# Kernel tuning notes

Measured on AMD Instinct MI355X. Metric: run time of the kernel, lower is better.

The kernel has to match this reference:

```python
import jax, jax.numpy as jnp
import numpy as np

N, E, F, H, HEADS, G = 50000, 800000, 128, 128, 4, 512
BN_EPS = 1e-5

def setup_inputs() -> dict:
    key = jax.random.key(0)
    ks = jax.random.split(key, 12)
    x = jax.random.normal(ks[0], (N, F), jnp.float32)
    edge_index = jax.random.randint(ks[1], (2, E), 0, N, jnp.int64)
    batch = jnp.sort(jax.random.randint(ks[2], (N,), 0, G, jnp.int64))
    w_gcn = jax.random.normal(ks[3], (F, H), jnp.float32) * 0.09
    b_gcn = jnp.zeros((H,), jnp.float32)
    g2_gamma = jnp.ones((H,), jnp.float32); g2_beta = jnp.zeros((H,), jnp.float32)
    g2_mean = jnp.zeros((H,), jnp.float32); g2_var = jnp.ones((H,), jnp.float32)
    w_gat = jax.random.normal(ks[4], (H, HEADS * H), jnp.float32) * 0.09
    a_src = jax.random.normal(ks[5], (HEADS, H), jnp.float32) * 0.1
    a_dst = jax.random.normal(ks[6], (HEADS, H), jnp.float32) * 0.1
    b_gat = jnp.zeros((HEADS * H,), jnp.float32)
    g1_gamma = jnp.ones((HEADS * H,), jnp.float32); g1_beta = jnp.zeros((HEADS * H,), jnp.float32)
    g1_mean = jnp.zeros((HEADS * H,), jnp.float32); g1_var = jnp.ones((HEADS * H,), jnp.float32)
    w_lin = jax.random.normal(ks[7], (12 * H, 16), jnp.float32) * 0.02
    b_lin = jnp.zeros((16,), jnp.float32)
    return dict(x=x, edge_index=edge_index, batch=batch, w_gcn=w_gcn, b_gcn=b_gcn,
                g2_gamma=g2_gamma, g2_beta=g2_beta, g2_mean=g2_mean, g2_var=g2_var,
                w_gat=w_gat, a_src=a_src, a_dst=a_dst, b_gat=b_gat,
                g1_gamma=g1_gamma, g1_beta=g1_beta, g1_mean=g1_mean, g1_var=g1_var,
                w_lin=w_lin, b_lin=b_lin)

def _bn_eval(h, gamma, beta, mean, var):
    return (h - mean) * jax.lax.rsqrt(var + BN_EPS) * gamma + beta

def _forward(x, src2, dst2, batch, w_gcn, b_gcn, g2_gamma, g2_beta, g2_mean, g2_var,
             w_gat, a_src, a_dst, b_gat, g1_gamma, g1_beta, g1_mean, g1_var, w_lin, b_lin):
    # ---- GCNConv (conv1) with self-loops, symmetric normalization ----
    h = x @ w_gcn                                   # [N,H]
    deg = jax.ops.segment_sum(jnp.ones_like(src2, dtype=h.dtype), dst2, N)
    dis = jax.lax.rsqrt(jnp.maximum(deg, 1.0))      # deg >= 1 due to self loops
    norm = dis[src2] * dis[dst2]                    # [E2]
    h = jax.ops.segment_sum(h[src2] * norm[:, None], dst2, N) + b_gcn
    # ---- BatchNorm (norm2, eval) + ReLU ----
    h = jax.nn.relu(_bn_eval(h, g2_gamma, g2_beta, g2_mean, g2_var))
    # ---- GATConv (gat2), heads=4 concat, self-loops, eval (no dropout) ----
    hg = (h @ w_gat).reshape(N, HEADS, H)           # [N,heads,H]
    asrc = jnp.einsum('nhd,hd->nh', hg, a_src)      # [N,heads]
    adst = jnp.einsum('nhd,hd->nh', hg, a_dst)
    e = jax.nn.leaky_relu(asrc[src2] + adst[dst2], 0.2)   # [E2,heads]
    emax = jax.ops.segment_max(e, dst2, N)                # all nodes covered by self-loops
    ex = jnp.exp(e - emax[dst2])
    esum = jax.ops.segment_sum(ex, dst2, N)
    alpha = ex / (esum[dst2] + 1e-16)                     # segment softmax over incoming edges
    out = jax.ops.segment_sum(hg[src2] * alpha[:, :, None], dst2, N)
    out = out.reshape(N, HEADS * H) + b_gat
    # ---- BatchNorm (norm1, eval) + ReLU ----
    out = jax.nn.relu(_bn_eval(out, g1_gamma, g1_beta, g1_mean, g1_var))
    # ---- global add / max / mean pooling over graphs ----
    sadd = jax.ops.segment_sum(out, batch, G)
    cnt = jax.ops.segment_sum(jnp.ones((N, 1), out.dtype), batch, G)
    smean = sadd / jnp.maximum(cnt, 1.0)
    smax = jax.ops.segment_max(out, batch, G)
    smax = jnp.where(cnt > 0, smax, 0.0)
    feat = jnp.concatenate([sadd, smax, smean], axis=1)   # [G, 12*H]
    return jax.nn.sigmoid(feat @ w_lin + b_lin)

def reference(x, edge_index, batch, w_gcn, b_gcn, g2_gamma, g2_beta, g2_mean, g2_var,
              w_gat, a_src, a_dst, b_gat, g1_gamma, g1_beta, g1_mean, g1_var, w_lin, b_lin):
    sl = jnp.arange(N, dtype=edge_index.dtype)
    src2 = jnp.concatenate([edge_index[0], sl])
    dst2 = jnp.concatenate([edge_index[1], sl])
    return _forward(x, src2, dst2, batch, w_gcn, b_gcn, g2_gamma, g2_beta, g2_mean, g2_var,
                    w_gat, a_src, a_dst, b_gat, g1_gamma, g1_beta, g1_mean, g1_var, w_lin, b_lin)
```

## Files before the change

kernel.cpp:

```cpp
#include <hip/hip_runtime.h>

#define NN 50000
#define NE 800000
#define NE2 (NE + NN)
#define CSRN (NE + 2 * NN)
#define FD 128
#define HD 128
#define NHD 4
#define OD 512
#define NG 512
#define BN_EPS 1e-5f

#define SCAN_CHUNK 2048
#define EB_CHUNK 4096
#define NB_F ((NE + EB_CHUNK - 1) / EB_CHUNK)
#define NBUCK ((NN + 511) / 512)
#define NH (NBUCK * NB_F)
#define NB2 ((NH + SCAN_CHUNK - 1) / SCAN_CHUNK)
#define CAPR 13312

#define XB_BLOCKS (NN * FD / 4 / 256)
#define WG_BLOCKS (FD * HD / 256)
#define WA_BLOCKS (HD * OD / 256)
#define CP_XB0 7
#define CP_WG0 (CP_XB0 + XB_BLOCKS)
#define CP_WA0 (CP_WG0 + WG_BLOCKS)
#define CP_Z0  (CP_WA0 + WA_BLOCKS)
#define CP_GS0 (CP_Z0 + 1)
#define CP_FZ0 (CP_GS0 + 3)
#define CP_NB  (CP_FZ0 + 768)

typedef __attribute__((ext_vector_type(8))) short bfrag;
typedef __attribute__((ext_vector_type(4))) float f32x4;
typedef __attribute__((ext_vector_type(2))) float f32x2;
typedef unsigned short ushort_t;

__device__ inline ushort_t f2bf(float f) {
    unsigned int u = __float_as_uint(f);
    unsigned int r = (u + 0x7fffu + ((u >> 16) & 1u)) >> 16;
    return (ushort_t)r;
}
__device__ inline float bf2f_lo(unsigned int v) { return __uint_as_float(v << 16); }
__device__ inline float bf2f_hi(unsigned int v) { return __uint_as_float(v & 0xffff0000u); }

__global__ __launch_bounds__(256) void histA_k(const int* __restrict__ ei,
                                               int* __restrict__ hist) {
    __shared__ int h[NBUCK];
    int blk = blockIdx.x, t = threadIdx.x;
    for (int i = t; i < NBUCK; i += 256) h[i] = 0;
    __syncthreads();
    int e0 = blk * EB_CHUNK;
    for (int i = t; i < EB_CHUNK; i += 256) {
        int e = e0 + i;
        if (e < NE) atomicAdd(&h[ei[NE + e] >> 9], 1);
    }
    __syncthreads();
    for (int i = t; i < NBUCK; i += 256) hist[i * NB_F + blk] = h[i];
}

__global__ __launch_bounds__(256) void scanA2_k(const int* __restrict__ hist,
                                                int* __restrict__ bsum2) {
    __shared__ int red[256];
    int b = blockIdx.x, t = threadIdx.x;
    int base = b * SCAN_CHUNK + t * 8;
    int s = 0;
    #pragma unroll
    for (int i = 0; i < 8; ++i) { int idx = base + i; if (idx < NH) s += hist[idx]; }
    red[t] = s;
    __syncthreads();
    for (int off = 128; off; off >>= 1) {
        if (t < off) red[t] += red[t + off];
        __syncthreads();
    }
    if (t == 0) bsum2[b] = red[0];
}

__global__ __launch_bounds__(256) void scanC2_k(const int* __restrict__ hist,
                                                const int* __restrict__ bsum2,
                                                int* __restrict__ base) {
    __shared__ int red[256];
    __shared__ int boff_s;
    int b = blockIdx.x, t = threadIdx.x;
    if (t == 0) {
        int run = 0;
        for (int i = 0; i < b; ++i) run += bsum2[i];
        boff_s = run;
    }
    int bse = b * SCAN_CHUNK + t * 8;
    int v[8];
    int s = 0;
    #pragma unroll
    for (int i = 0; i < 8; ++i) {
        int idx = bse + i;
        v[i] = (idx < NH) ? hist[idx] : 0;
        s += v[i];
    }
    red[t] = s;
    __syncthreads();
    for (int off = 1; off < 256; off <<= 1) {
        int y = (t >= off) ? red[t - off] : 0;
        __syncthreads();
        red[t] += y;
        __syncthreads();
    }
    int run = boff_s + red[t] - s;
    #pragma unroll
    for (int i = 0; i < 8; ++i) {
        int idx = bse + i;
        if (idx < NH) { base[idx] = run; run += v[i]; }
    }
    if (b == 0 && t == 0) base[NH] = NE;
}

__global__ __launch_bounds__(256) void scatter2_k(const int* __restrict__ ei,
                                                  const int* __restrict__ base,
                                                  int2* __restrict__ ebuf) {
    __shared__ int cur[NBUCK];
    int blk = blockIdx.x, t = threadIdx.x;
    for (int i = t; i < NBUCK; i += 256) cur[i] = base[i * NB_F + blk];
    __syncthreads();
    int e0 = blk * EB_CHUNK;
    for (int i = t; i < EB_CHUNK; i += 256) {
        int e = e0 + i;
        if (e < NE) {
            int src = ei[e], dst = ei[NE + e];
            int pos = atomicAdd(&cur[dst >> 9], 1);
            ebuf[pos] = make_int2(src, dst);
        }
    }
}

__global__ __launch_bounds__(256) void bfill_k(const int2* __restrict__ ebuf,
                                               const int* __restrict__ base,
                                               int* __restrict__ rowptr,
                                               float* __restrict__ dis,
                                               int* __restrict__ csr) {
    __shared__ int cnt[512];
    __shared__ int pref[512];
    __shared__ int red[256];
    __shared__ int stage[CAPR];
    int b = blockIdx.x, t = threadIdx.x;
    int n0 = b * 512;
    int nn = min(512, NN - n0);
    int eb0 = base[b * NB_F];
    int eb1 = base[(b + 1) * NB_F];
    int ecnt = eb1 - eb0;
    int gbase = eb0 + 2 * n0;
    for (int i = t; i < nn; i += 256) cnt[i] = 0;
    __syncthreads();
    for (int e = eb0 + t; e < eb1; e += 256)
        atomicAdd(&cnt[ebuf[e].y - n0], 1);
    __syncthreads();
    int i0 = 2 * t, i1 = 2 * t + 1;
    int v0 = (i0 < nn) ? cnt[i0] + 2 : 0;
    int v1 = (i1 < nn) ? cnt[i1] + 2 : 0;
    int ps = v0 + v1;
    red[t] = ps;
    __syncthreads();
    for (int off = 1; off < 256; off <<= 1) {
        int y = (t >= off) ? red[t - off] : 0;
        __syncthreads();
        red[t] += y;
        __syncthreads();
    }
    int excl = red[t] - ps;
    if (i0 < nn) pref[i0] = excl;
    if (i1 < nn) pref[i1] = excl + v0;
    __syncthreads();
    int region = ecnt + 2 * nn;
    for (int i = t; i < nn; i += 256) {
        rowptr[n0 + i] = gbase + pref[i];
        dis[n0 + i] = rsqrtf((float)(cnt[i] + 1));
    }
    if (b == 0 && t == 0) rowptr[NN] = CSRN;
    __syncthreads();
    for (int i = t; i < nn; i += 256) cnt[i] = 0;
    __syncthreads();
    if (region <= CAPR) {
        for (int i = t; i < nn; i += 256) {
            int r = pref[i];
            stage[r] = 0;
            stage[r + 1] = n0 + i;
        }
        __syncthreads();
        for (int e = eb0 + t; e < eb1; e += 256) {
            int2 ed = ebuf[e];
            int l = ed.y - n0;
            int pos = atomicAdd(&cnt[l], 1);
            stage[pref[l] + 2 + pos] = ed.x;
        }
        __syncthreads();
        for (int i = t; i < region; i += 256) csr[gbase + i] = stage[i];
    } else {
        for (int i = t; i < nn; i += 256) {
            int r = gbase + pref[i];
            csr[r] = 0;
            csr[r + 1] = n0 + i;
        }
        __syncthreads();
        for (int e = eb0 + t; e < eb1; e += 256) {
            int2 ed = ebuf[e];
            int l = ed.y - n0;
            int pos = atomicAdd(&cnt[l], 1);
            csr[gbase + pref[l] + 2 + pos] = ed.x;
        }
    }
}

__global__ __launch_bounds__(256) void castprep_k(
    const float* __restrict__ b_gcn, const float* __restrict__ g2_gam,
    const float* __restrict__ g2_bet, const float* __restrict__ g2_mean,
    const float* __restrict__ g2_var, const float* __restrict__ b_gat,
    const float* __restrict__ g1_gam, const float* __restrict__ g1_bet,
    const float* __restrict__ g1_mean, const float* __restrict__ g1_var,
    float* __restrict__ Ag, float* __restrict__ Bg,
    float* __restrict__ Aa, float* __restrict__ Ba,
    const float* __restrict__ a_src, const float* __restrict__ a_dst,
    float* __restrict__ waT,
    const float* __restrict__ x, ushort_t* __restrict__ xb,
    const float* __restrict__ w_gcn, ushort_t* __restrict__ wgT,
    const float* __restrict__ w_gat, ushort_t* __restrict__ wgatT,
    ushort_t* __restrict__ h0b, const int* __restrict__ batch,
    int* __restrict__ gstart, float* __restrict__ feat) {
    int b = blockIdx.x, tid = threadIdx.x;
    if (b < 3) {
        int t = b * 256 + tid;
        if (t < HD) {
            float a = rsqrtf(g2_var[t] + BN_EPS) * g2_gam[t];
            Ag[t] = a;
            Bg[t] = (b_gcn[t] - g2_mean[t]) * a + g2_bet[t];
        } else if (t < HD + OD) {
            int d = t - HD;
            float a = rsqrtf(g1_var[d] + BN_EPS) * g1_gam[d];
            Aa[d] = a;
            Ba[d] = (b_gat[d] - g1_mean[d]) * a + g1_bet[d];
        }
    } else if (b < 7) {
        int t = (b - 3) * 256 + tid;
        int k = t >> 3, j = t & 7, head = j & 3;
        const float* av = (j < 4 ? a_src : a_dst) + head * 128;
        const float* w = w_gat + (size_t)k * OD + head * 128;
        float s = 0.f;
        for (int d = 0; d < 128; ++d) s += w[d] * av[d];
        waT[j * 128 + k] = s;
    } else if (b < CP_WG0) {
        int t = (b - CP_XB0) * 256 + tid;
        float4 v = ((const float4*)x)[t];
        ushort_t o[4] = {f2bf(v.x), f2bf(v.y), f2bf(v.z), f2bf(v.w)};
        *(unsigned long long*)(xb + 4 * t) = *(unsigned long long*)o;
    } else if (b < CP_WA0) {
        int t = (b - CP_WG0) * 256 + tid;
        int n = t / FD, k = t - n * FD;
        wgT[n * FD + k] = f2bf(w_gcn[k * HD + n]);
    } else if (b < CP_Z0) {
        int t = (b - CP_WA0) * 256 + tid;
        int n = t / HD, k = t - n * HD;
        wgatT[n * HD + k] = f2bf(w_gat[k * OD + n]);
    } else if (b < CP_GS0) {
        if (tid < 64) ((unsigned int*)(h0b + (size_t)NN * HD))[tid] = 0u;
    } else if (b < CP_FZ0) {
        int g = (b - CP_GS0) * 256 + tid;
        if (g <= NG) {
            int lo = 0, hi = NN;
            while (lo < hi) { int mid = (lo + hi) >> 1; if (batch[mid] < g) lo = mid + 1; else hi = mid; }
            gstart[g] = lo;
        }
    } else {
        int t = (b - CP_FZ0) * 256 + tid;
        float4 z = make_float4(0.f, 0.f, 0.f, 0.f);
        *(float4*)(feat + 4 * (size_t)t) = z;
    }
}

template <bool SCALE>
__global__ __launch_bounds__(256) void gemm_bf16_t(const ushort_t* __restrict__ A,
                                                   const ushort_t* __restrict__ BT,
                                                   const float* __restrict__ rowscale,
                                                   ushort_t* __restrict__ C,
                                                   int M, int N) {
    __shared__ short As[128][136];
    __shared__ short Bs[64][136];
    const int tid = threadIdx.x;
    const int m0 = blockIdx.x * 128;
    const int n0 = blockIdx.y * 64;

    #pragma unroll
    for (int i = 0; i < 8; ++i) {
        int c = tid + 256 * i;
        int row = c >> 4, off = (c & 15) * 8;
        bfrag v = (bfrag)0;
        if (m0 + row < M) v = *(const bfrag*)(A + (size_t)(m0 + row) * 128 + off);
        *(bfrag*)&As[row][off] = v;
    }
    #pragma unroll
    for (int i = 0; i < 4; ++i) {
        int c = tid + 256 * i;
        int row = c >> 4, off = (c & 15) * 8;
        *(bfrag*)&Bs[row][off] = *(const bfrag*)(BT + (size_t)(n0 + row) * 128 + off);
    }
    __syncthreads();

    const int w = tid >> 6;
    const int lr = tid & 15;
    const int kg = (tid & 63) >> 4;

    f32x4 acc[2][4];
    #pragma unroll
    for (int mi = 0; mi < 2; ++mi)
        #pragma unroll
        for (int ni = 0; ni < 4; ++ni) acc[mi][ni] = (f32x4)0.f;

    #pragma unroll
    for (int ks = 0; ks < 4; ++ks) {
        bfrag af[2], bb[4];
        #pragma unroll
        for (int mi = 0; mi < 2; ++mi)
            af[mi] = *(const bfrag*)&As[32 * w + 16 * mi + lr][32 * ks + 8 * kg];
        #pragma unroll
        for (int ni = 0; ni < 4; ++ni)
            bb[ni] = *(const bfrag*)&Bs[16 * ni + lr][32 * ks + 8 * kg];
        #pragma unroll
        for (int mi = 0; mi < 2; ++mi)
            #pragma unroll
            for (int ni = 0; ni < 4; ++ni)
                acc[mi][ni] = __builtin_amdgcn_mfma_f32_16x16x32_bf16(
                    af[mi], bb[ni], acc[mi][ni], 0, 0, 0);
    }

    #pragma unroll
    for (int mi = 0; mi < 2; ++mi) {
        #pragma unroll
        for (int r = 0; r < 4; ++r) {
            int row = m0 + 32 * w + 16 * mi + 4 * kg + r;
            if (row < M) {
                float sc = SCALE ? rowscale[row] : 1.f;
                #pragma unroll
                for (int ni = 0; ni < 4; ++ni) {
                    int col = n0 + 16 * ni + lr;
                    float v = acc[mi][ni][r];
                    if (SCALE) v *= sc;
                    C[(size_t)row * N + col] = f2bf(v);
                }
            }
        }
    }
}

__global__ __launch_bounds__(256) void gemm_zp_k(const ushort_t* __restrict__ zb,
                                                 const ushort_t* __restrict__ wgatT,
                                                 const float* __restrict__ Aa,
                                                 const float* __restrict__ Ba,
                                                 const int* __restrict__ batch,
                                                 const int* __restrict__ gstart,
                                                 float* __restrict__ feat) {
    __shared__ short As[128][136];
    __shared__ short Bs[64][136];
    const int tid = threadIdx.x;
    const int head = blockIdx.z;
    const int m0 = blockIdx.x * 128;
    const int n0 = blockIdx.y * 64;
    const ushort_t* A = zb + (size_t)head * NN * HD;
    const ushort_t* BT = wgatT + (size_t)head * HD * HD;

    #pragma unroll
    for (int i = 0; i < 8; ++i) {
        int c = tid + 256 * i;
        int row = c >> 4, off = (c & 15) * 8;
        bfrag v = (bfrag)0;
        if (m0 + row < NN) v = *(const bfrag*)(A + (size_t)(m0 + row) * HD + off);
        *(bfrag*)&As[row][off] = v;
    }
    #pragma unroll
    for (int i = 0; i < 4; ++i) {
        int c = tid + 256 * i;
        int row = c >> 4, off = (c & 15) * 8;
        *(bfrag*)&Bs[row][off] = *(const bfrag*)(BT + (size_t)(n0 + row) * HD + off);
    }
    __syncthreads();

    const int w = tid >> 6;
    const int lr = tid & 15;
    const int kg = (tid & 63) >> 4;

    f32x4 acc[2][4];
    #pragma unroll
    for (int mi = 0; mi < 2; ++mi)
        #pragma unroll
        for (int ni = 0; ni < 4; ++ni) acc[mi][ni] = (f32x4)0.f;

    #pragma unroll
    for (int ks = 0; ks < 4; ++ks) {
        bfrag af[2], bb[4];
        #pragma unroll
        for (int mi = 0; mi < 2; ++mi)
            af[mi] = *(const bfrag*)&As[32 * w + 16 * mi + lr][32 * ks + 8 * kg];
        #pragma unroll
        for (int ni = 0; ni < 4; ++ni)
            bb[ni] = *(const bfrag*)&Bs[16 * ni + lr][32 * ks + 8 * kg];
        #pragma unroll
        for (int mi = 0; mi < 2; ++mi)
            #pragma unroll
            for (int ni = 0; ni < 4; ++ni)
                acc[mi][ni] = __builtin_amdgcn_mfma_f32_16x16x32_bf16(
                    af[mi], bb[ni], acc[mi][ni], 0, 0, 0);
    }

    __syncthreads();
    float (*vals)[65] = reinterpret_cast<float(*)[65]>(&As[0][0]);
    float (*psum)[64] = reinterpret_cast<float(*)[64]>(&Bs[0][0]);
    float (*pmax)[64] = reinterpret_cast<float(*)[64]>(&Bs[8][0]);

    #pragma unroll
    for (int mi = 0; mi < 2; ++mi) {
        #pragma unroll
        for (int r = 0; r < 4; ++r) {
            int lrow = 32 * w + 16 * mi + 4 * kg + r;
            int row = m0 + lrow;
            if (row < NN) {
                #pragma unroll
                for (int ni = 0; ni < 4; ++ni) {
                    int gc = 128 * head + n0 + 16 * ni + lr;
                    float v = fmaf(acc[mi][ni][r], Aa[gc], Ba[gc]);
                    vals[lrow][16 * ni + lr] = fmaxf(v, 0.f);
                }
            }
        }
    }
    __syncthreads();

    int rmax = min(128, NN - m0);
    int gfirst = batch[m0];
    int glast = batch[m0 + rmax - 1];
    int c = tid & 63, part = tid >> 6;
    for (int gg = gfirst; gg <= glast; ++gg) {
        int s = max(gstart[gg], m0) - m0;
        int e = min(gstart[gg + 1], m0 + rmax) - m0;
        float sm = 0.f, mx = 0.f;
        for (int r = s + part; r < e; r += 4) {
            float v = vals[r][c];
            sm += v;
            mx = fmaxf(mx, v);
        }
        psum[part][c] = sm;
        pmax[part][c] = mx;
        __syncthreads();
        if (part == 0) {
            float ts = (psum[0][c] + psum[1][c]) + (psum[2][c] + psum[3][c]);
            float tm = fmaxf(fmaxf(pmax[0][c], pmax[1][c]), fmaxf(pmax[2][c], pmax[3][c]));
            if (e > s) {
                int gc = 128 * head + n0 + c;
                atomicAdd(&feat[(size_t)gg * 1536 + gc], ts);
                atomicMax((int*)&feat[(size_t)gg * 1536 + 512 + gc], __float_as_int(tm));
            }
        }
        __syncthreads();
    }
}

__global__ __launch_bounds__(256) void gcn_agg4_k(
    const ushort_t* __restrict__ h0, const int* __restrict__ rowptr,
    const int* __restrict__ csr, const float* __restrict__ dis,
    const float* __restrict__ Ag, const float* __restrict__ Bg,
    const float* __restrict__ waT,
    ushort_t* __restrict__ h, float* __restrict__ asrc, float* __restrict__ adst) {
    int lane = threadIdx.x & 63;
    int g = lane >> 4;
    int sl = lane & 15;
    int sl8 = sl * 8;
    int n = __builtin_amdgcn_readfirstlane((int)(blockIdx.x * 4) + (int)(threadIdx.x >> 6));
    int r0 = __builtin_amdgcn_readfirstlane(rowptr[n]) + 1;
    int r1 = __builtin_amdgcn_readfirstlane(rowptr[n + 1]);
    const uint4* h0_u4 = (const uint4*)h0;
    f32x2 a2[4];
    #pragma unroll
    for (int q = 0; q < 4; ++q) a2[q] = (f32x2)0.f;
    uint4 hv[2];

#define GLOAD(i, BASE) { int _e = (BASE) + g; int _sv = csr[_e]; \
    int _s = _e < r1 ? _sv : NN; \
    hv[i] = h0_u4[(unsigned)_s * 16u + (unsigned)sl]; }
#define GACC(i) { \
    f32x2 _f0 = {bf2f_lo(hv[i].x), bf2f_hi(hv[i].x)}; \
    f32x2 _f1 = {bf2f_lo(hv[i].y), bf2f_hi(hv[i].y)}; \
    f32x2 _f2 = {bf2f_lo(hv[i].z), bf2f_hi(hv[i].z)}; \
    f32x2 _f3 = {bf2f_lo(hv[i].w), bf2f_hi(hv[i].w)}; \
    a2[0] += _f0; a2[1] += _f1; a2[2] += _f2; a2[3] += _f3; }

    GLOAD(0, r0) GLOAD(1, r0 + 4)
    for (int base = r0; base < r1; base += 8) {
        GACC(0) GLOAD(0, base + 8)
        GACC(1) GLOAD(1, base + 12)
    }
#undef GLOAD
#undef GACC

    #pragma unroll
    for (int q = 0; q < 4; ++q) {
        f32x2 v = a2[q];
        v.x += __shfl_xor(v.x, 16); v.x += __shfl_xor(v.x, 32);
        v.y += __shfl_xor(v.y, 16); v.y += __shfl_xor(v.y, 32);
        a2[q] = v;
    }
    float a[8] = {a2[0].x, a2[0].y, a2[1].x, a2[1].y,
                  a2[2].x, a2[2].y, a2[3].x, a2[3].y};
    float t = dis[n];
    float4 A0 = *(const float4*)(Ag + sl8);
    float4 A1 = *(const float4*)(Ag + sl8 + 4);
    float4 B0 = *(const float4*)(Bg + sl8);
    float4 B1 = *(const float4*)(Bg + sl8 + 4);
    float o[8];
    o[0] = fmaxf(fmaf(a[0] * t, A0.x, B0.x), 0.f);
    o[1] = fmaxf(fmaf(a[1] * t, A0.y, B0.y), 0.f);
    o[2] = fmaxf(fmaf(a[2] * t, A0.z, B0.z), 0.f);
    o[3] = fmaxf(fmaf(a[3] * t, A0.w, B0.w), 0.f);
    o[4] = fmaxf(fmaf(a[4] * t, A1.x, B1.x), 0.f);
    o[5] = fmaxf(fmaf(a[5] * t, A1.y, B1.y), 0.f);
    o[6] = fmaxf(fmaf(a[6] * t, A1.z, B1.z), 0.f);
    o[7] = fmaxf(fmaf(a[7] * t, A1.w, B1.w), 0.f);
    if (g == 0) {
        uint4 pk;
        pk.x = (unsigned int)f2bf(o[0]) | ((unsigned int)f2bf(o[1]) << 16);
        pk.y = (unsigned int)f2bf(o[2]) | ((unsigned int)f2bf(o[3]) << 16);
        pk.z = (unsigned int)f2bf(o[4]) | ((unsigned int)f2bf(o[5]) << 16);
        pk.w = (unsigned int)f2bf(o[6]) | ((unsigned int)f2bf(o[7]) << 16);
        *(uint4*)(h + (size_t)n * HD + sl8) = pk;
    }
    const float* w0p = waT + (2 * g) * 128 + sl8;
    const float* w1p = waT + (2 * g + 1) * 128 + sl8;
    float4 wA0 = *(const float4*)(w0p);
    float4 wA1 = *(const float4*)(w0p + 4);
    float4 wB0 = *(const float4*)(w1p);
    float4 wB1 = *(const float4*)(w1p + 4);
    float p0 = o[0] * wA0.x + o[1] * wA0.y + o[2] * wA0.z + o[3] * wA0.w
             + o[4] * wA1.x + o[5] * wA1.y + o[6] * wA1.z + o[7] * wA1.w;
    float p1 = o[0] * wB0.x + o[1] * wB0.y + o[2] * wB0.z + o[3] * wB0.w
             + o[4] * wB1.x + o[5] * wB1.y + o[6] * wB1.z + o[7] * wB1.w;
    #pragma unroll
    for (int off2 = 1; off2 < 16; off2 <<= 1) {
        p0 += __shfl_xor(p0, off2);
        p1 += __shfl_xor(p1, off2);
    }
    if (sl == 0) {
        int j0 = 2 * g;
        float* d0 = (j0 < 4) ? asrc : adst;
        float* d1 = (j0 + 1 < 4) ? asrc : adst;
        d0[n * 4 + (j0 & 3)] = p0;
        d1[n * 4 + ((j0 + 1) & 3)] = p1;
    }
}

__global__ __launch_bounds__(256) void zgather3_k(
    const ushort_t* __restrict__ h, const int* __restrict__ rowptr,
    const int* __restrict__ csr, const float* __restrict__ asrc,
    const float* __restrict__ adst, ushort_t* __restrict__ zb) {
    __shared__ float4 p4s[4][64];
    __shared__ int sis[4][64];
    int wv = threadIdx.x >> 6;
    int lane = threadIdx.x & 63;
    int g = lane >> 4;
    int sl = lane & 15;
    int sl8 = sl * 8;
    int n = __builtin_amdgcn_readfirstlane((int)(blockIdx.x * 4) + wv);
    int r0 = __builtin_amdgcn_readfirstlane(rowptr[n]) + 1;
    int r1 = __builtin_amdgcn_readfirstlane(rowptr[n + 1]);
    const uint4* h_u4 = (const uint4*)h;
    float4 ad = *(const float4*)(adst + 4 * n);

    f32x2 acc[4][4];
    #pragma unroll
    for (int hh = 0; hh < 4; ++hh)
        #pragma unroll
        for (int q = 0; q < 4; ++q) acc[hh][q] = (f32x2)0.f;
    f32x2 s01 = (f32x2)0.f, s23 = (f32x2)0.f;

    uint4 hv[2];
    f32x2 pa[2], pb[2];

#define ZLOAD(i, ST) { int _idx = min((ST) * 4 + g, 63); \
    float4 _p = p4s[wv][_idx]; \
    int _s = sis[wv][_idx]; \
    pa[i].x = _p.x; pa[i].y = _p.y; pb[i].x = _p.z; pb[i].y = _p.w; \
    hv[i] = h_u4[(unsigned)_s * 16u + (unsigned)sl]; }
#define ZACC(i) { \
    f32x2 _f0 = {bf2f_lo(hv[i].x), bf2f_hi(hv[i].x)}; \
    f32x2 _f1 = {bf2f_lo(hv[i].y), bf2f_hi(hv[i].y)}; \
    f32x2 _f2 = {bf2f_lo(hv[i].z), bf2f_hi(hv[i].z)}; \
    f32x2 _f3 = {bf2f_lo(hv[i].w), bf2f_hi(hv[i].w)}; \
    s01 += pa[i]; s23 += pb[i]; \
    f32x2 _p0 = {pa[i].x, pa[i].x}; \
    f32x2 _p1 = {pa[i].y, pa[i].y}; \
    f32x2 _p2 = {pb[i].x, pb[i].x}; \
    f32x2 _p3 = {pb[i].y, pb[i].y}; \
    acc[0][0] = __builtin_elementwise_fma(_p0, _f0, acc[0][0]); \
    acc[0][1] = __builtin_elementwise_fma(_p0, _f1, acc[0][1]); \
    acc[0][2] = __builtin_elementwise_fma(_p0, _f2, acc[0][2]); \
    acc[0][3] = __builtin_elementwise_fma(_p0, _f3, acc[0][3]); \
    acc[1][0] = __builtin_elementwise_fma(_p1, _f0, acc[1][0]); \
    acc[1][1] = __builtin_elementwise_fma(_p1, _f1, acc[1][1]); \
    acc[1][2] = __builtin_elementwise_fma(_p1, _f2, acc[1][2]); \
    acc[1][3] = __builtin_elementwise_fma(_p1, _f3, acc[1][3]); \
    acc[2][0] = __builtin_elementwise_fma(_p2, _f0, acc[2][0]); \
    acc[2][1] = __builtin_elementwise_fma(_p2, _f1, acc[2][1]); \
    acc[2][2] = __builtin_elementwise_fma(_p2, _f2, acc[2][2]); \
    acc[2][3] = __builtin_elementwise_fma(_p2, _f3, acc[2][3]); \
    acc[3][0] = __builtin_elementwise_fma(_p3, _f0, acc[3][0]); \
    acc[3][1] = __builtin_elementwise_fma(_p3, _f1, acc[3][1]); \
    acc[3][2] = __builtin_elementwise_fma(_p3, _f2, acc[3][2]); \
    acc[3][3] = __builtin_elementwise_fma(_p3, _f3, acc[3][3]); }

    for (int base = r0; base < r1; base += 64) {
        {
            int e = base + lane;
            bool v = e < r1;
            int sv = csr[e];
            int s = v ? sv : 0;
            float4 as = *(const float4*)(asrc + 4 * (size_t)s);
            f32x2 x01 = {as.x + ad.x, as.y + ad.y};
            f32x2 x23 = {as.z + ad.z, as.w + ad.w};
            f32x2 l01 = __builtin_elementwise_max(x01, 0.2f * x01);
            f32x2 l23 = __builtin_elementwise_max(x23, 0.2f * x23);
            float4 p;
            p.x = v ? __expf(l01.x) : 0.f;
            p.y = v ? __expf(l01.y) : 0.f;
            p.z = v ? __expf(l23.x) : 0.f;
            p.w = v ? __expf(l23.y) : 0.f;
            p4s[wv][lane] = p;
            sis[wv][lane] = s;
        }
        int rem = r1 - base; if (rem > 64) rem = 64;
        int nsteps = (rem + 3) >> 2;
        ZLOAD(0, 0) ZLOAD(1, 1)
        for (int st = 0; st < nsteps; st += 2) {
            ZACC(0) ZLOAD(0, st + 2)
            ZACC(1) ZLOAD(1, st + 3)
        }
    }
#undef ZLOAD
#undef ZACC

    bool gb0 = (g & 1) != 0;
    bool gb1 = (g & 2) != 0;
    f32x2 tot[4];
    #pragma unroll
    for (int q = 0; q < 4; ++q) {
        f32x2 sA = gb0 ? acc[0][q] : acc[1][q];
        f32x2 sB = gb0 ? acc[2][q] : acc[3][q];
        f32x2 rA, rB;
        rA.x = __shfl_xor(sA.x, 16); rA.y = __shfl_xor(sA.y, 16);
        rB.x = __shfl_xor(sB.x, 16); rB.y = __shfl_xor(sB.y, 16);
        f32x2 kA = (gb0 ? acc[1][q] : acc[0][q]) + rA;
        f32x2 kB = (gb0 ? acc[3][q] : acc[2][q]) + rB;
        f32x2 s2 = gb1 ? kA : kB;
        f32x2 r2;
        r2.x = __shfl_xor(s2.x, 32); r2.y = __shfl_xor(s2.y, 32);
        tot[q] = (gb1 ? kB : kA) + r2;
    }
    float sA1 = gb0 ? s01.x : s01.y;
    float sB1 = gb0 ? s23.x : s23.y;
    float rA1 = __shfl_xor(sA1, 16);
    float rB1 = __shfl_xor(sB1, 16);
    float kAs = (gb0 ? s01.y : s01.x) + rA1;
    float kBs = (gb0 ? s23.y : s23.x) + rB1;
    float s2s = gb1 ? kAs : kBs;
    float r2s = __shfl_xor(s2s, 32);
    float stot = (gb1 ? kBs : kAs) + r2s;
    float invg = 1.f / (stot + 1e-16f);

    unsigned int pkc[4];
    #pragma unroll
    for (int q = 0; q < 4; ++q) {
        f32x2 v = tot[q] * invg;
        pkc[q] = (unsigned int)f2bf(v.x) | ((unsigned int)f2bf(v.y) << 16);
    }
    uint4 pk = {pkc[0], pkc[1], pkc[2], pkc[3]};
    *(uint4*)(zb + (size_t)g * NN * HD + (size_t)n * HD + sl8) = pk;
}

__global__ __launch_bounds__(256) void head2_k(const float* __restrict__ feat,
                                               const int* __restrict__ gstart,
                                               const float* __restrict__ w_lin,
                                               const float* __restrict__ b_lin,
                                               float* __restrict__ out) {
    __shared__ float fs[1536];
    __shared__ float red[256];
    int g = blockIdx.x, t = threadIdx.x;
    int cnt = gstart[g + 1] - gstart[g];
    float inv = cnt > 0 ? 1.f / (float)cnt : 0.f;
    for (int i = t; i < 512; i += 256) {
        float sa = feat[(size_t)g * 1536 + i];
        float mx = feat[(size_t)g * 1536 + 512 + i];
        fs[i] = sa;
        fs[512 + i] = mx;
        fs[1024 + i] = sa * inv;
    }
    __syncthreads();
    int o = t & 15, part = t >> 4;
    float s = 0.f;
    int kbeg = part * 96;
    for (int k = kbeg; k < kbeg + 96; ++k) s += fs[k] * w_lin[k * 16 + o];
    red[t] = s;
    __syncthreads();
    if (t < 16) {
        float tot = b_lin[o];
        for (int p = 0; p < 16; ++p) tot += red[p * 16 + o];
        out[g * 16 + o] = 1.f / (1.f + __expf(-tot));
    }
}

extern "C" void kernel_launch(void* const* d_in, const int* in_sizes, int n_in,
                              void* d_out, int out_size, void* d_ws, size_t ws_size,
                              hipStream_t stream) {
    const float* x       = (const float*)d_in[0];
    const int*   ei      = (const int*)d_in[1];
    const int*   batch   = (const int*)d_in[2];
    const float* w_gcn   = (const float*)d_in[3];
    const float* b_gcn   = (const float*)d_in[4];
    const float* g2_gam  = (const float*)d_in[5];
    const float* g2_bet  = (const float*)d_in[6];
    const float* g2_mean = (const float*)d_in[7];
    const float* g2_var  = (const float*)d_in[8];
    const float* w_gat   = (const float*)d_in[9];
    const float* a_src   = (const float*)d_in[10];
    const float* a_dst   = (const float*)d_in[11];
    const float* b_gat   = (const float*)d_in[12];
    const float* g1_gam  = (const float*)d_in[13];
    const float* g1_bet  = (const float*)d_in[14];
    const float* g1_mean = (const float*)d_in[15];
    const float* g1_var  = (const float*)d_in[16];
    const float* w_lin   = (const float*)d_in[17];
    const float* b_lin   = (const float*)d_in[18];
    float* out = (float*)d_out;

    char* ws = (char*)d_ws;
    size_t off = 0;
    auto alloc = [&](size_t bytes) -> void* {
        void* p = ws + off;
        off += (bytes + 255) & ~(size_t)255;
        return p;
    };
    int* hist       = (int*)alloc((size_t)NH * 4);
    int* bsum2      = (int*)alloc((size_t)NB2 * 4);
    int* base       = (int*)alloc((size_t)(NH + 1) * 4);
    int2* ebuf      = (int2*)alloc((size_t)NE * 8);
    int* rowptr     = (int*)alloc((size_t)(NN + 1) * 4);
    int* csr        = (int*)alloc((size_t)(CSRN + 64) * 4);
    int* gstart     = (int*)alloc((size_t)(NG + 1) * 4);
    float* dis      = (float*)alloc((size_t)NN * 4);
    ushort_t* xb    = (ushort_t*)alloc((size_t)NN * FD * 2);
    ushort_t* wgT   = (ushort_t*)alloc((size_t)FD * HD * 2);
    ushort_t* wgatT = (ushort_t*)alloc((size_t)HD * OD * 2);
    ushort_t* h0b   = (ushort_t*)alloc((size_t)(NN + 1) * HD * 2);
    ushort_t* hb    = (ushort_t*)alloc((size_t)NN * HD * 2);
    ushort_t* zb    = (ushort_t*)alloc((size_t)NHD * NN * HD * 2);
    float* asrc     = (float*)alloc((size_t)NN * 4 * 4);
    float* adst     = (float*)alloc((size_t)NN * 4 * 4);
    float* waT      = (float*)alloc((size_t)8 * 128 * 4);
    float* Ag       = (float*)alloc((size_t)HD * 4);
    float* Bg       = (float*)alloc((size_t)HD * 4);
    float* Aa       = (float*)alloc((size_t)OD * 4);
    float* Ba       = (float*)alloc((size_t)OD * 4);
    float* feat     = (float*)alloc((size_t)NG * 1536 * 4);

    histA_k<<<NB_F, 256, 0, stream>>>(ei, hist);
    scanA2_k<<<NB2, 256, 0, stream>>>(hist, bsum2);
    scanC2_k<<<NB2, 256, 0, stream>>>(hist, bsum2, base);
    scatter2_k<<<NB_F, 256, 0, stream>>>(ei, base, ebuf);
    bfill_k<<<NBUCK, 256, 0, stream>>>(ebuf, base, rowptr, dis, csr);

    castprep_k<<<CP_NB, 256, 0, stream>>>(
        b_gcn, g2_gam, g2_bet, g2_mean, g2_var,
        b_gat, g1_gam, g1_bet, g1_mean, g1_var,
        Ag, Bg, Aa, Ba, a_src, a_dst, waT,
        x, xb, w_gcn, wgT, w_gat, wgatT, h0b, batch, gstart, feat);

    gemm_bf16_t<true><<<dim3((NN + 127) / 128, HD / 64), 256, 0, stream>>>(
        xb, wgT, dis, h0b, NN, HD);

    gcn_agg4_k<<<NN / 4, 256, 0, stream>>>(h0b, rowptr, csr, dis, Ag, Bg, waT,
                                           hb, asrc, adst);

    zgather3_k<<<NN / 4, 256, 0, stream>>>(hb, rowptr, csr, asrc, adst, zb);

    gemm_zp_k<<<dim3((NN + 127) / 128, HD / 64, NHD), 256, 0, stream>>>(
        zb, wgatT, Aa, Ba, batch, gstart, feat);

    head2_k<<<NG, 256, 0, stream>>>(feat, gstart, w_lin, b_lin, out);
}
```

Baseline: 189.4 us.

## Fuse fp32-to-bf16 cast of x into GCN GEMM; stage CSR indices in LDS

Removes the separate conversion of x to bf16 in the prep kernel. The first GEMM now loads fp32 x directly and converts it while filling shared memory, which avoids writing and re-reading the bf16 copy of x. Because the GEMM grid has two column blocks, x is now read twice in fp32. Separately, the GCN aggregation kernel loads source indices in batches of 64 into shared memory with one coalesced read per wave, then gathers rows from LDS-held indices instead of issuing a scalar CSR load per gather step.

```diff
diff --git a/kernel.cpp b/kernel.cpp
--- a/kernel.cpp
+++ b/kernel.cpp
@@ -19,16 +19,14 @@
 #define NB2 ((NH + SCAN_CHUNK - 1) / SCAN_CHUNK)
 #define CAPR 13312
 
-#define XB_BLOCKS (NN * FD / 4 / 256)
 #define WG_BLOCKS (FD * HD / 256)
 #define WA_BLOCKS (HD * OD / 256)
-#define CP_XB0 7
-#define CP_WG0 (CP_XB0 + XB_BLOCKS)
-#define CP_WA0 (CP_WG0 + WG_BLOCKS)
-#define CP_Z0  (CP_WA0 + WA_BLOCKS)
-#define CP_GS0 (CP_Z0 + 1)
-#define CP_FZ0 (CP_GS0 + 3)
-#define CP_NB  (CP_FZ0 + 768)
+#define CP_WGT0 7
+#define CP_WGATT0 (CP_WGT0 + WG_BLOCKS)
+#define CP_ZROW (CP_WGATT0 + WA_BLOCKS)
+#define CP_GST0 (CP_ZROW + 1)
+#define CP_FZ0 (CP_GST0 + 3)
+#define CP_NB (CP_FZ0 + 768)
 
 typedef __attribute__((ext_vector_type(8))) short bfrag;
 typedef __attribute__((ext_vector_type(4))) float f32x4;
@@ -217,7 +215,6 @@
     float* __restrict__ Aa, float* __restrict__ Ba,
     const float* __restrict__ a_src, const float* __restrict__ a_dst,
     float* __restrict__ waT,
-    const float* __restrict__ x, ushort_t* __restrict__ xb,
     const float* __restrict__ w_gcn, ushort_t* __restrict__ wgT,
     const float* __restrict__ w_gat, ushort_t* __restrict__ wgatT,
     ushort_t* __restrict__ h0b, const int* __restrict__ batch,
@@ -243,23 +240,18 @@
         float s = 0.f;
         for (int d = 0; d < 128; ++d) s += w[d] * av[d];
         waT[j * 128 + k] = s;
-    } else if (b < CP_WG0) {
-        int t = (b - CP_XB0) * 256 + tid;
-        float4 v = ((const float4*)x)[t];
-        ushort_t o[4] = {f2bf(v.x), f2bf(v.y), f2bf(v.z), f2bf(v.w)};
-        *(unsigned long long*)(xb + 4 * t) = *(unsigned long long*)o;
-    } else if (b < CP_WA0) {
-        int t = (b - CP_WG0) * 256 + tid;
+    } else if (b < CP_WGATT0) {
+        int t = (b - CP_WGT0) * 256 + tid;
         int n = t / FD, k = t - n * FD;
         wgT[n * FD + k] = f2bf(w_gcn[k * HD + n]);
-    } else if (b < CP_Z0) {
-        int t = (b - CP_WA0) * 256 + tid;
+    } else if (b < CP_ZROW) {
+        int t = (b - CP_WGATT0) * 256 + tid;
         int n = t / HD, k = t - n * HD;
         wgatT[n * HD + k] = f2bf(w_gat[k * OD + n]);
-    } else if (b < CP_GS0) {
+    } else if (b == CP_ZROW) {
         if (tid < 64) ((unsigned int*)(h0b + (size_t)NN * HD))[tid] = 0u;
     } else if (b < CP_FZ0) {
-        int g = (b - CP_GS0) * 256 + tid;
+        int g = (b - CP_GST0) * 256 + tid;
         if (g <= NG) {
             int lo = 0, hi = NN;
             while (lo < hi) { int mid = (lo + hi) >> 1; if (batch[mid] < g) lo = mid + 1; else hi = mid; }
@@ -272,12 +264,11 @@
     }
 }
 
-template <bool SCALE>
-__global__ __launch_bounds__(256) void gemm_bf16_t(const ushort_t* __restrict__ A,
-                                                   const ushort_t* __restrict__ BT,
-                                                   const float* __restrict__ rowscale,
-                                                   ushort_t* __restrict__ C,
-                                                   int M, int N) {
+__global__ __launch_bounds__(256) void gemm_x_k(const float* __restrict__ A,
+                                                const ushort_t* __restrict__ BT,
+                                                const float* __restrict__ rowscale,
+                                                ushort_t* __restrict__ C,
+                                                int M, int N) {
     __shared__ short As[128][136];
     __shared__ short Bs[64][136];
     const int tid = threadIdx.x;
@@ -285,12 +276,13 @@
     const int n0 = blockIdx.y * 64;
 
     #pragma unroll
-    for (int i = 0; i < 8; ++i) {
+    for (int i = 0; i < 16; ++i) {
         int c = tid + 256 * i;
-        int row = c >> 4, off = (c & 15) * 8;
-        bfrag v = (bfrag)0;
-        if (m0 + row < M) v = *(const bfrag*)(A + (size_t)(m0 + row) * 128 + off);
-        *(bfrag*)&As[row][off] = v;
+        int row = c >> 5, off = (c & 31) * 4;
+        float4 v = make_float4(0.f, 0.f, 0.f, 0.f);
+        if (m0 + row < M) v = *(const float4*)(A + (size_t)(m0 + row) * 128 + off);
+        ushort_t o[4] = {f2bf(v.x), f2bf(v.y), f2bf(v.z), f2bf(v.w)};
+        *(unsigned long long*)&As[row][off] = *(unsigned long long*)o;
     }
     #pragma unroll
     for (int i = 0; i < 4; ++i) {
@@ -333,13 +325,11 @@
         for (int r = 0; r < 4; ++r) {
             int row = m0 + 32 * w + 16 * mi + 4 * kg + r;
             if (row < M) {
-                float sc = SCALE ? rowscale[row] : 1.f;
+                float sc = rowscale[row];
                 #pragma unroll
                 for (int ni = 0; ni < 4; ++ni) {
                     int col = n0 + 16 * ni + lr;
-                    float v = acc[mi][ni][r];
-                    if (SCALE) v *= sc;
-                    C[(size_t)row * N + col] = f2bf(v);
+                    C[(size_t)row * N + col] = f2bf(acc[mi][ni][r] * sc);
                 }
             }
         }
@@ -463,11 +453,13 @@
     const float* __restrict__ Ag, const float* __restrict__ Bg,
     const float* __restrict__ waT,
     ushort_t* __restrict__ h, float* __restrict__ asrc, float* __restrict__ adst) {
+    __shared__ int sis2[4][64];
+    int wv = threadIdx.x >> 6;
     int lane = threadIdx.x & 63;
     int g = lane >> 4;
     int sl = lane & 15;
     int sl8 = sl * 8;
-    int n = __builtin_amdgcn_readfirstlane((int)(blockIdx.x * 4) + (int)(threadIdx.x >> 6));
+    int n = __builtin_amdgcn_readfirstlane((int)(blockIdx.x * 4) + wv);
     int r0 = __builtin_amdgcn_readfirstlane(rowptr[n]) + 1;
     int r1 = __builtin_amdgcn_readfirstlane(rowptr[n + 1]);
     const uint4* h0_u4 = (const uint4*)h0;
@@ -476,8 +468,8 @@
     for (int q = 0; q < 4; ++q) a2[q] = (f32x2)0.f;
     uint4 hv[2];
 
-#define GLOAD(i, BASE) { int _e = (BASE) + g; int _sv = csr[_e]; \
-    int _s = _e < r1 ? _sv : NN; \
+#define GLOAD(i, ST) { int _idx = min((ST) * 4 + g, 63); \
+    int _s = sis2[wv][_idx]; \
     hv[i] = h0_u4[(unsigned)_s * 16u + (unsigned)sl]; }
 #define GACC(i) { \
     f32x2 _f0 = {bf2f_lo(hv[i].x), bf2f_hi(hv[i].x)}; \
@@ -486,10 +478,19 @@
     f32x2 _f3 = {bf2f_lo(hv[i].w), bf2f_hi(hv[i].w)}; \
     a2[0] += _f0; a2[1] += _f1; a2[2] += _f2; a2[3] += _f3; }
 
-    GLOAD(0, r0) GLOAD(1, r0 + 4)
-    for (int base = r0; base < r1; base += 8) {
-        GACC(0) GLOAD(0, base + 8)
-        GACC(1) GLOAD(1, base + 12)
+    for (int base = r0; base < r1; base += 64) {
+        {
+            int e = base + lane;
+            int sv = csr[e];
+            sis2[wv][lane] = (e < r1) ? sv : NN;
+        }
+        int rem = r1 - base; if (rem > 64) rem = 64;
+        int nsteps = (rem + 3) >> 2;
+        GLOAD(0, 0) GLOAD(1, 1)
+        for (int st = 0; st < nsteps; st += 2) {
+            GACC(0) GLOAD(0, st + 2)
+            GACC(1) GLOAD(1, st + 3)
+        }
     }
 #undef GLOAD
 #undef GACC
@@ -746,7 +747,6 @@
     int* csr        = (int*)alloc((size_t)(CSRN + 64) * 4);
     int* gstart     = (int*)alloc((size_t)(NG + 1) * 4);
     float* dis      = (float*)alloc((size_t)NN * 4);
-    ushort_t* xb    = (ushort_t*)alloc((size_t)NN * FD * 2);
     ushort_t* wgT   = (ushort_t*)alloc((size_t)FD * HD * 2);
     ushort_t* wgatT = (ushort_t*)alloc((size_t)HD * OD * 2);
     ushort_t* h0b   = (ushort_t*)alloc((size_t)(NN + 1) * HD * 2);
@@ -771,10 +771,10 @@
         b_gcn, g2_gam, g2_bet, g2_mean, g2_var,
         b_gat, g1_gam, g1_bet, g1_mean, g1_var,
         Ag, Bg, Aa, Ba, a_src, a_dst, waT,
-        x, xb, w_gcn, wgT, w_gat, wgatT, h0b, batch, gstart, feat);
-
-    gemm_bf16_t<true><<<dim3((NN + 127) / 128, HD / 64), 256, 0, stream>>>(
-        xb, wgT, dis, h0b, NN, HD);
+        w_gcn, wgT, w_gat, wgatT, h0b, batch, gstart, feat);
+
+    gemm_x_k<<<dim3((NN + 127) / 128, HD / 64), 256, 0, stream>>>(
+        x, wgT, dis, h0b, NN, HD);
 
     gcn_agg4_k<<<NN / 4, 256, 0, stream>>>(h0b, rowptr, csr, dis, Ag, Bg, waT,
                                            hb, asrc, adst);
```

Result: slower. 193.6 us (+2.2%).
